# Kernel tuning notes

Hardware: AMD Instinct MI355X
Metric: run time of the kernel (lower is better)

The kernel has to match this reference:

```python
import jax, jax.numpy as jnp
import numpy as np

N_EMBD = 1024
HEAD_SIZE = 128
B, T = 8, 4096


def setup_inputs() -> dict:
    key = jax.random.key(0)
    ks = jax.random.split(key, 7)
    s = 1.0 / np.sqrt(N_EMBD)
    return {
        "x": jax.random.normal(ks[0], (B, T, N_EMBD), dtype=jnp.float32),
        "Wq": jax.random.uniform(ks[1], (N_EMBD, HEAD_SIZE), jnp.float32, -s, s),
        "bq": jax.random.uniform(ks[2], (HEAD_SIZE,), jnp.float32, -s, s),
        "Wk": jax.random.uniform(ks[3], (N_EMBD, HEAD_SIZE), jnp.float32, -s, s),
        "bk": jax.random.uniform(ks[4], (HEAD_SIZE,), jnp.float32, -s, s),
        "Wv": jax.random.uniform(ks[5], (N_EMBD, HEAD_SIZE), jnp.float32, -s, s),
        "bv": jax.random.uniform(ks[6], (HEAD_SIZE,), jnp.float32, -s, s),
    }


def reference(x, Wq, bq, Wk, bk, Wv, bv):
    # q,k,v: [B,T,H]
    q = x @ Wq + bq
    k = x @ Wk + bk
    v = x @ Wv + bv
    scale = HEAD_SIZE ** -0.5
    att = jnp.einsum("bth,bsh->bts", q, k) * scale  # [B,T,T]
    t = x.shape[1]
    causal = jnp.tril(jnp.ones((t, t), dtype=bool))
    att = jnp.where(causal, att, -jnp.inf)
    att = jax.nn.softmax(att, axis=-1)
    # dropout with p=0.0 is identity (eval-mode equivalent)
    out = jnp.einsum("bts,bsh->bth", att, v)  # [B,T,H]
    return out
```

## Files before the change

### kernel.cpp

```cpp
#include <hip/hip_runtime.h>
#include <hip/hip_bf16.h>
#include <stdint.h>

#define BATCH 8
#define SEQ   4096
#define EMB   1024
#define HD    128
#define NROWS 32768

typedef __attribute__((ext_vector_type(8))) short short8;
typedef __attribute__((ext_vector_type(4))) float f32x4;

__device__ inline unsigned short f2bf(float f) {
    union { float f; unsigned int u; } c; c.f = f;
    unsigned int u = c.u;
    unsigned int r = (u + 0x7fffu + ((u >> 16) & 1u)) >> 16;
    return (unsigned short)r;
}
__device__ inline float bf2f(unsigned short u) {
    union { unsigned int i; float f; } c; c.i = ((unsigned int)u) << 16; return c.f;
}
__device__ inline unsigned int pkbf(float a, float b) {
    __hip_bfloat162 h = __float22bfloat162_rn(make_float2(a, b));
    union { __hip_bfloat162 h; unsigned int u; } c; c.h = h; return c.u;
}

#define GLDS16(gp, lp) __builtin_amdgcn_global_load_lds( \
    (const __attribute__((address_space(1))) void*)(gp), \
    (__attribute__((address_space(3))) void*)(lp), 16, 0, 0)

__device__ inline void decomp(int it, int& b, int& qt, int& kv) {
    b = it / 1056;
    int r = it - b * 1056;
    int q = (int)((__builtin_sqrtf(4.0f * (float)r + 1.0f) - 1.0f) * 0.5f);
    while ((q + 1) * (q + 2) <= r) ++q;
    while (q * (q + 1) > r) --q;
    qt = q;
    kv = r - q * (q + 1);
}
__device__ inline int chunk_of(int I) {
    return (I < 4352) ? (I / 17) : (256 + ((I - 4352) >> 4));
}
__device__ inline int base1(int qt) {
    if (qt < 8)  return qt;
    if (qt < 16) return 8 + 2 * (qt - 8);
    if (qt < 24) return 24 + 3 * (qt - 16);
    return 48 + 4 * (qt - 24);
}

__global__ __launch_bounds__(256) void prep_kernel(
    const float* __restrict__ Wq, const float* __restrict__ bq,
    const float* __restrict__ Wk, const float* __restrict__ bk,
    const float* __restrict__ Wv, const float* __restrict__ bv,
    unsigned short* __restrict__ wt, float* __restrict__ biasc)
{
    const int n = blockIdx.x;
    const int sel = n >> 7, h = n & 127;
    const float* W = (sel == 0) ? Wq : (sel == 1) ? Wk : Wv;
    const int tid = threadIdx.x;
    const int k0 = tid * 4;
    union { unsigned short us[4]; uint2 v; } pk;
#pragma unroll
    for (int u = 0; u < 4; ++u) pk.us[u] = f2bf(W[(size_t)(k0 + u) * HD + h]);
    *(uint2*)&wt[(size_t)n * EMB + k0] = pk.v;
    if (tid == 0) {
        const float* bp = (sel == 0) ? bq : (sel == 1) ? bk : bv;
        biasc[n] = bp[h];
    }
}

__global__ __launch_bounds__(768, 3) void gemm_qkv(
    const float* __restrict__ x, const unsigned short* __restrict__ wt,
    const float* __restrict__ biasc,
    unsigned short* __restrict__ q, unsigned short* __restrict__ kOut,
    unsigned short* __restrict__ vt)
{
    const int m0  = blockIdx.x * 128;
    const int tid = threadIdx.x;
    const int wave = tid >> 6, lane = tid & 63;
    const int quad = lane >> 4, l15 = lane & 15;
    const int wm = (wave >= 6) ? 1 : 0;
    const int wn = wave - wm * 6;

    __shared__ __align__(16) unsigned short As[2][128][40];
    __shared__ __align__(16) unsigned short Bs[2][12288];

    f32x4 acc[4][4];
#pragma unroll
    for (int i = 0; i < 4; ++i)
#pragma unroll
        for (int j = 0; j < 4; ++j) acc[i][j] = (f32x4){0.f, 0.f, 0.f, 0.f};

    const int aactive = (tid < 512);
    const int arow = tid >> 3, akc = (tid & 7) * 4;
    float4 aR0, aR1;

#define LOAD_A(kt)                                                          \
    if (aactive) {                                                          \
        aR0 = *(const float4*)(x + (size_t)(m0 + arow) * EMB + (kt) * 32 + akc);        \
        aR1 = *(const float4*)(x + (size_t)(m0 + arow + 64) * EMB + (kt) * 32 + akc);   \
    }
#define WRITE_A(buf)                                                        \
    if (aactive) {                                                          \
        union { unsigned short us[4]; uint2 v; } p0, p1;                    \
        p0.us[0] = f2bf(aR0.x); p0.us[1] = f2bf(aR0.y);                     \
        p0.us[2] = f2bf(aR0.z); p0.us[3] = f2bf(aR0.w);                     \
        *(uint2*)&As[buf][arow][akc] = p0.v;                                \
        p1.us[0] = f2bf(aR1.x); p1.us[1] = f2bf(aR1.y);                     \
        p1.us[2] = f2bf(aR1.z); p1.us[3] = f2bf(aR1.w);                     \
        *(uint2*)&As[buf][arow + 64][akc] = p1.v;                           \
    }
#define STAGE_B(kt, buf)                                                    \
    {                                                                       \
        _Pragma("unroll")                                                   \
        for (int g = 0; g < 2; ++g) {                                       \
            int s0 = (g * 12 + wave) * 64;                                  \
            int s  = s0 + lane;                                             \
            int n  = s >> 2, c = (s & 3) ^ (n & 3);                         \
            GLDS16(wt + (size_t)n * EMB + (kt) * 32 + c * 8,                \
                   &Bs[buf][s0 * 8]);                                       \
        }                                                                   \
    }

    LOAD_A(0); STAGE_B(0, 0); WRITE_A(0);
    int cur = 0;

    for (int kt = 0; kt < 32; ++kt) {
        __syncthreads();
        if (kt < 31) { LOAD_A(kt + 1); STAGE_B(kt + 1, cur ^ 1); }
        short8 af[4], bw[4];
#pragma unroll
        for (int mj = 0; mj < 4; ++mj)
            af[mj] = *(const short8*)&As[cur][wm * 64 + mj * 16 + l15][quad * 8];
#pragma unroll
        for (int ni = 0; ni < 4; ++ni) {
            int n = wn * 64 + ni * 16 + l15;
            bw[ni] = *(const short8*)&Bs[cur][n * 32 + ((quad ^ (n & 3)) << 3)];
        }
#pragma unroll
        for (int ni = 0; ni < 4; ++ni)
#pragma unroll
            for (int mj = 0; mj < 4; ++mj)
                acc[ni][mj] = __builtin_amdgcn_mfma_f32_16x16x32_bf16(
                    bw[ni], af[mj], acc[ni][mj], 0, 0, 0);
        if (kt < 31) WRITE_A(cur ^ 1);
        cur ^= 1;
    }

    const float qscale = 0.08838834764831845f * 1.4426950408889634f;
    const int bb = m0 >> 12;
    const int t0 = m0 & 4095;
    const int mrow0 = m0 + wm * 64;
    const int tl0   = t0 + wm * 64;
#pragma unroll
    for (int ni = 0; ni < 4; ++ni) {
        int colbase = wn * 64 + ni * 16;
        int sel = colbase >> 7;
        int c0 = colbase + quad * 4;
        float4 bv4 = *(const float4*)&biasc[c0];
#pragma unroll
        for (int mj = 0; mj < 4; ++mj) {
            int m = mrow0 + mj * 16 + l15;
            if (sel == 0) {
                union { unsigned short us[4]; uint2 v; } pk;
#pragma unroll
                for (int j = 0; j < 4; ++j)
                    pk.us[j] = f2bf((acc[ni][mj][j] + ((const float*)&bv4)[j]) * qscale);
                *(uint2*)&q[(size_t)m * HD + (c0 & 127)] = pk.v;
            } else if (sel == 1) {
                union { unsigned short us[4]; uint2 v; } pk;
#pragma unroll
                for (int j = 0; j < 4; ++j)
                    pk.us[j] = f2bf(acc[ni][mj][j] + ((const float*)&bv4)[j]);
                *(uint2*)&kOut[(size_t)m * HD + (c0 & 127)] = pk.v;
            } else {
#pragma unroll
                for (int j = 0; j < 4; ++j) {
                    int h = (c0 & 127) + j;
                    vt[((size_t)(bb * 128 + h)) * SEQ + tl0 + mj * 16 + l15] =
                        f2bf(acc[ni][mj][j] + ((const float*)&bv4)[j]);
                }
            }
        }
    }
#undef LOAD_A
#undef WRITE_A
#undef STAGE_B
}

__global__ __launch_bounds__(256, 2) void attn_kernel(
    const unsigned short* __restrict__ q, const unsigned short* __restrict__ k,
    const unsigned short* __restrict__ vt, float* __restrict__ out,
    float* __restrict__ Oseg, float2* __restrict__ ml)
{
    const int rank  = blockIdx.x;
    const int start = (rank < 256) ? 17 * rank : 4352 + ((rank - 256) << 4);
    const int iend  = start + ((rank < 256) ? 17 : 16);

    const int tid  = threadIdx.x;
    const int wave = tid >> 6, lane = tid & 63;
    const int quad = lane >> 4, l15 = lane & 15;

    __shared__ __align__(16) unsigned short Ks[2][8192];
    __shared__ __align__(16) unsigned short Vs[2][8192];

    const int bpa0 = (l15 + 16 * ((2 * quad) & 3)) * 4;
    const int bpa1 = (l15 + 16 * ((2 * quad + 1) & 3)) * 4;

#define STAGE_KV(b_, kv_, buf_)                                              \
    {                                                                        \
        const size_t kb0 = (size_t)(b_) * SEQ + (kv_) * 64;                  \
        const size_t vb0 = (size_t)(b_) * HD * SEQ + (kv_) * 64;             \
        _Pragma("unroll")                                                    \
        for (int g = 0; g < 4; ++g) {                                        \
            int s0 = (g * 4 + wave) * 64;                                    \
            int s  = s0 + lane;                                              \
            int key = s >> 4, c = (s & 15) ^ (key & 15);                     \
            GLDS16(k + (kb0 + key) * HD + c * 8, &Ks[buf_][s0 * 8]);         \
        }                                                                    \
        _Pragma("unroll")                                                    \
        for (int g = 0; g < 4; ++g) {                                        \
            int s0 = (g * 4 + wave) * 64;                                    \
            int s  = s0 + lane;                                              \
            int h = s >> 3, c = (s & 7) ^ (h & 7);                           \
            GLDS16(vt + vb0 + (size_t)h * SEQ + c * 8, &Vs[buf_][s0 * 8]);   \
        }                                                                    \
    }

    int b, qt, kv;
    decomp(start, b, qt, kv);

    short8 qf[2][4];
    f32x4  o[2][8];
    float  m_r[2], l_r[2];
    int    qrow0 = 0;

#define CTX_INIT(b_, q_)                                                     \
    {                                                                        \
        qrow0 = (q_) * 128 + wave * 32;                                      \
        const size_t qoff = (size_t)(b_) * SEQ + qrow0;                      \
        _Pragma("unroll")                                                    \
        for (int mi = 0; mi < 2; ++mi)                                       \
            _Pragma("unroll")                                                \
            for (int kh = 0; kh < 4; ++kh)                                   \
                qf[mi][kh] = *(const short8*)(q + (qoff + mi * 16 + l15) * HD + kh * 32 + quad * 8); \
        _Pragma("unroll")                                                    \
        for (int mi = 0; mi < 2; ++mi) {                                     \
            _Pragma("unroll")                                                \
            for (int hi = 0; hi < 8; ++hi) o[mi][hi] = (f32x4){0.f, 0.f, 0.f, 0.f}; \
            m_r[mi] = -1e30f; l_r[mi] = 0.f;                                 \
        }                                                                    \
    }

#define CTX_FLUSH()                                                          \
    {                                                                        \
        const int I0 = b * 1056 + qt * (qt + 1);                             \
        const int j  = rank - chunk_of(I0);                                  \
        const int rr = wave * 32;                                            \
        float* obase;                                                        \
        if (j == 0) obase = out + ((size_t)b * SEQ + qrow0) * HD;            \
        else obase = Oseg + ((size_t)(b * 80 + base1(qt) + j - 1) * 128 + rr) * HD; \
        const size_t mlb = ((size_t)(b * 32 + qt) * 5 + j) * 128 + rr;       \
        _Pragma("unroll")                                                    \
        for (int mi = 0; mi < 2; ++mi) {                                     \
            if (quad == 0) ml[mlb + mi * 16 + l15] = make_float2(m_r[mi], l_r[mi]); \
            _Pragma("unroll")                                                \
            for (int hi = 0; hi < 8; ++hi)                                   \
                *(f32x4*)&obase[(size_t)(mi * 16 + l15) * HD + hi * 16 + quad * 4] = o[mi][hi]; \
        }                                                                    \
    }

    STAGE_KV(b, kv, 0);
    CTX_INIT(b, qt);
    int cur = 0;

    for (int it = start; it < iend; ++it) {
        int b2 = 0, qt2 = 0, kv2 = 0;
        const bool more = (it + 1 < iend);
        if (more) decomp(it + 1, b2, qt2, kv2);

        __syncthreads();
        if (more) STAGE_KV(b2, kv2, cur ^ 1);

        const int key0 = kv * 64;
        f32x4 s[2][4];
#pragma unroll
        for (int mi = 0; mi < 2; ++mi)
#pragma unroll
            for (int ni = 0; ni < 4; ++ni) s[mi][ni] = (f32x4){0.f, 0.f, 0.f, 0.f};
        __builtin_amdgcn_s_setprio(1);
#pragma unroll
        for (int kh = 0; kh < 4; ++kh) {
#pragma unroll
            for (int ni = 0; ni < 4; ++ni) {
                short8 kf = *(const short8*)&Ks[cur][(ni * 16 + l15) * 128 + (((kh * 4 + quad) ^ l15) << 3)];
                s[0][ni] = __builtin_amdgcn_mfma_f32_16x16x32_bf16(kf, qf[0][kh], s[0][ni], 0, 0, 0);
                s[1][ni] = __builtin_amdgcn_mfma_f32_16x16x32_bf16(kf, qf[1][kh], s[1][ni], 0, 0, 0);
            }
        }
        __builtin_amdgcn_s_setprio(0);
        if (key0 + 63 > qrow0) {
#pragma unroll
            for (int mi = 0; mi < 2; ++mi)
#pragma unroll
                for (int ni = 0; ni < 4; ++ni)
#pragma unroll
                    for (int j = 0; j < 4; ++j) {
                        int key = key0 + ni * 16 + quad * 4 + j;
                        int t   = qrow0 + mi * 16 + l15;
                        if (key > t) s[mi][ni][j] = -1e30f;
                    }
        }
        unsigned int pk[2][4][2];
#pragma unroll
        for (int mi = 0; mi < 2; ++mi) {
            float mx = -1e30f;
#pragma unroll
            for (int ni = 0; ni < 4; ++ni)
#pragma unroll
                for (int j = 0; j < 4; ++j) mx = fmaxf(mx, s[mi][ni][j]);
            mx = fmaxf(mx, __shfl_xor(mx, 16));
            mx = fmaxf(mx, __shfl_xor(mx, 32));
            if (!__all(mx - m_r[mi] <= 8.0f)) {
                float mnew = fmaxf(m_r[mi], mx);
                float alpha = __builtin_amdgcn_exp2f(m_r[mi] - mnew);
                m_r[mi] = mnew;
                l_r[mi] *= alpha;
#pragma unroll
                for (int hi = 0; hi < 8; ++hi) o[mi][hi] *= alpha;
            }
            const float mcur = m_r[mi];
            float rs = 0.f;
#pragma unroll
            for (int ni = 0; ni < 4; ++ni) {
                float p0 = __builtin_amdgcn_exp2f(s[mi][ni][0] - mcur);
                float p1 = __builtin_amdgcn_exp2f(s[mi][ni][1] - mcur);
                float p2 = __builtin_amdgcn_exp2f(s[mi][ni][2] - mcur);
                float p3 = __builtin_amdgcn_exp2f(s[mi][ni][3] - mcur);
                rs += (p0 + p1) + (p2 + p3);
                pk[mi][ni][0] = pkbf(p0, p1);
                pk[mi][ni][1] = pkbf(p2, p3);
            }
            rs += __shfl_xor(rs, 16);
            rs += __shfl_xor(rs, 32);
            l_r[mi] += rs;
        }
        short8 pT[2][2];
#pragma unroll
        for (int mi = 0; mi < 2; ++mi)
#pragma unroll
            for (int sk = 0; sk < 2; ++sk) {
                union { unsigned int u[4]; short8 s8; } pt;
                int lo = 2 * sk, hi_ = 2 * sk + 1;
                unsigned int a0 = (unsigned)__builtin_amdgcn_ds_bpermute(bpa0, (int)pk[mi][lo][0]);
                unsigned int b0 = (unsigned)__builtin_amdgcn_ds_bpermute(bpa0, (int)pk[mi][hi_][0]);
                pt.u[0] = (quad < 2) ? a0 : b0;
                unsigned int a1 = (unsigned)__builtin_amdgcn_ds_bpermute(bpa0, (int)pk[mi][lo][1]);
                unsigned int b1 = (unsigned)__builtin_amdgcn_ds_bpermute(bpa0, (int)pk[mi][hi_][1]);
                pt.u[1] = (quad < 2) ? a1 : b1;
                unsigned int a2 = (unsigned)__builtin_amdgcn_ds_bpermute(bpa1, (int)pk[mi][lo][0]);
                unsigned int b2 = (unsigned)__builtin_amdgcn_ds_bpermute(bpa1, (int)pk[mi][hi_][0]);
                pt.u[2] = (quad < 2) ? a2 : b2;
                unsigned int a3 = (unsigned)__builtin_amdgcn_ds_bpermute(bpa1, (int)pk[mi][lo][1]);
                unsigned int b3 = (unsigned)__builtin_amdgcn_ds_bpermute(bpa1, (int)pk[mi][hi_][1]);
                pt.u[3] = (quad < 2) ? a3 : b3;
                pT[mi][sk] = pt.s8;
            }
        __builtin_amdgcn_s_setprio(1);
#pragma unroll
        for (int sk = 0; sk < 2; ++sk)
#pragma unroll
            for (int hi = 0; hi < 8; ++hi) {
                short8 vf = *(const short8*)&Vs[cur][(hi * 16 + l15) * 64 + (((sk * 4 + quad) ^ (l15 & 7)) << 3)];
                o[0][hi] = __builtin_amdgcn_mfma_f32_16x16x32_bf16(vf, pT[0][sk], o[0][hi], 0, 0, 0);
                o[1][hi] = __builtin_amdgcn_mfma_f32_16x16x32_bf16(vf, pT[1][sk], o[1][hi], 0, 0, 0);
            }
        __builtin_amdgcn_s_setprio(0);

        if (kv == 2 * qt + 1 || !more) {
            CTX_FLUSH();
            if (more && kv == 2 * qt + 1) CTX_INIT(b2, qt2);
        }
        b = b2; qt = qt2; kv = kv2;
        cur ^= 1;
    }
#undef STAGE_KV
#undef CTX_INIT
#undef CTX_FLUSH
}

__global__ __launch_bounds__(256) void merge_kernel(
    float* __restrict__ out, const float* __restrict__ Oseg,
    const float2* __restrict__ ml)
{
    int idx = blockIdx.x * 256 + threadIdx.x;
    int row = idx >> 5;
    int hc  = (idx & 31) << 2;
    int b = row >> 12, t = row & 4095, qt = t >> 7, rr = t & 127;
    int I0  = b * 1056 + qt * (qt + 1);
    int nkv = 2 * (qt + 1);
    int c_lo = chunk_of(I0);
    int c_hi = chunk_of(I0 + nkv - 1);
    int nseg = c_hi - c_lo + 1;

    const float2* mlp = ml + ((size_t)(b * 32 + qt) * 5) * 128 + rr;
    float2 s0 = mlp[0];
    float M = s0.x;
    for (int j = 1; j < nseg; ++j) M = fmaxf(M, mlp[(size_t)j * 128].x);

    float w0 = __builtin_amdgcn_exp2f(s0.x - M);
    float L  = w0 * s0.y;
    f32x4 a = *(const f32x4*)&out[(size_t)row * HD + hc];
    a = a * w0;
    for (int j = 1; j < nseg; ++j) {
        float2 mj = mlp[(size_t)j * 128];
        float w = __builtin_amdgcn_exp2f(mj.x - M);
        L += w * mj.y;
        const float* sp = Oseg + ((size_t)(b * 80 + base1(qt) + j - 1) * 128 + rr) * HD + hc;
        f32x4 sv = *(const f32x4*)sp;
        a = a + sv * w;
    }
    float inv = 1.0f / L;
    *(f32x4*)&out[(size_t)row * HD + hc] = a * inv;
}

extern "C" void kernel_launch(void* const* d_in, const int* in_sizes, int n_in,
                              void* d_out, int out_size, void* d_ws, size_t ws_size,
                              hipStream_t stream) {
    const float* x  = (const float*)d_in[0];
    const float* Wq = (const float*)d_in[1];
    const float* bq = (const float*)d_in[2];
    const float* Wk = (const float*)d_in[3];
    const float* bk = (const float*)d_in[4];
    const float* Wv = (const float*)d_in[5];
    const float* bv = (const float*)d_in[6];
    float* out = (float*)d_out;

    unsigned short* wt    = (unsigned short*)d_ws;
    float*          biasc = (float*)((char*)d_ws + 786432);
    unsigned short* qb    = (unsigned short*)((char*)d_ws + 787968);
    unsigned short* kb    = qb  + (size_t)NROWS * HD;
    unsigned short* vtb   = kb  + (size_t)NROWS * HD;
    float*          Oseg  = (float*)((char*)d_ws + 787968 + 3ull * NROWS * HD * 2);
    float2*         mlseg = (float2*)((char*)Oseg + 640ull * 128 * HD * 4);

    prep_kernel<<<dim3(384), 256, 0, stream>>>(Wq, bq, Wk, bk, Wv, bv, wt, biasc);
    gemm_qkv<<<dim3(256), 768, 0, stream>>>(x, wt, biasc, qb, kb, vtb);
    attn_kernel<<<dim3(512), 256, 0, stream>>>(qb, kb, vtb, out, Oseg, mlseg);
    merge_kernel<<<dim3(NROWS * 32 / 256), 256, 0, stream>>>(out, Oseg, mlseg);
}
```

Before: 316.8 us.

## Halve KV tile to 32 keys and split causal attention across 768 blocks

The attention kernel now walks K/V in 32-key tiles instead of 64. The flattened work is redistributed into 768 equal chunks of 22 tiles, interleaved across block indices, with three blocks per CU allowed by launch bounds and half-size LDS buffers. Waves whose 32 query rows lie entirely before a key tile now skip that tile's compute, which trims masked work on diagonal tiles. In exchange each tile carries more sync and staging overhead, and the extra partial segments add work to the merge pass and to workspace traffic.

```diff
diff --git a/kernel.cpp b/kernel.cpp
--- a/kernel.cpp
+++ b/kernel.cpp
@@ -30,22 +30,21 @@
     (__attribute__((address_space(3))) void*)(lp), 16, 0, 0)
 
 __device__ inline void decomp(int it, int& b, int& qt, int& kv) {
-    b = it / 1056;
-    int r = it - b * 1056;
-    int q = (int)((__builtin_sqrtf(4.0f * (float)r + 1.0f) - 1.0f) * 0.5f);
-    while ((q + 1) * (q + 2) <= r) ++q;
-    while (q * (q + 1) > r) --q;
+    b = it / 2112;
+    int r = it - b * 2112;
+    int q = (int)((__builtin_sqrtf(2.0f * (float)r + 1.0f) - 1.0f) * 0.5f);
+    while (2 * (q + 1) * (q + 2) <= r) ++q;
+    while (2 * q * (q + 1) > r) --q;
     qt = q;
-    kv = r - q * (q + 1);
-}
-__device__ inline int chunk_of(int I) {
-    return (I < 4352) ? (I / 17) : (256 + ((I - 4352) >> 4));
+    kv = r - 2 * q * (q + 1);
 }
 __device__ inline int base1(int qt) {
-    if (qt < 8)  return qt;
-    if (qt < 16) return 8 + 2 * (qt - 8);
-    if (qt < 24) return 24 + 3 * (qt - 16);
-    return 48 + 4 * (qt - 24);
+    if (qt < 5)  return qt;
+    if (qt < 11) return 5 + 2 * (qt - 5);
+    if (qt < 16) return 17 + 3 * (qt - 11);
+    if (qt < 22) return 32 + 4 * (qt - 16);
+    if (qt < 27) return 56 + 5 * (qt - 22);
+    return 81 + 6 * (qt - 27);
 }
 
 __global__ __launch_bounds__(256) void prep_kernel(
@@ -188,41 +187,42 @@
 #undef STAGE_B
 }
 
-__global__ __launch_bounds__(256, 2) void attn_kernel(
+__global__ __launch_bounds__(256, 3) void attn_kernel(
     const unsigned short* __restrict__ q, const unsigned short* __restrict__ k,
     const unsigned short* __restrict__ vt, float* __restrict__ out,
     float* __restrict__ Oseg, float2* __restrict__ ml)
 {
     const int rank  = blockIdx.x;
-    const int start = (rank < 256) ? 17 * rank : 4352 + ((rank - 256) << 4);
-    const int iend  = start + ((rank < 256) ? 17 : 16);
+    const int chunk = (rank & 7) * 96 + (rank >> 3);
+    const int start = chunk * 22;
+    const int iend  = start + 22;
 
     const int tid  = threadIdx.x;
     const int wave = tid >> 6, lane = tid & 63;
     const int quad = lane >> 4, l15 = lane & 15;
 
-    __shared__ __align__(16) unsigned short Ks[2][8192];
-    __shared__ __align__(16) unsigned short Vs[2][8192];
+    __shared__ __align__(16) unsigned short Ks[2][4096];
+    __shared__ __align__(16) unsigned short Vs[2][4096];
 
     const int bpa0 = (l15 + 16 * ((2 * quad) & 3)) * 4;
     const int bpa1 = (l15 + 16 * ((2 * quad + 1) & 3)) * 4;
 
 #define STAGE_KV(b_, kv_, buf_)                                              \
     {                                                                        \
-        const size_t kb0 = (size_t)(b_) * SEQ + (kv_) * 64;                  \
-        const size_t vb0 = (size_t)(b_) * HD * SEQ + (kv_) * 64;             \
+        const size_t kb0 = (size_t)(b_) * SEQ + (kv_) * 32;                  \
+        const size_t vb0 = (size_t)(b_) * HD * SEQ + (kv_) * 32;             \
         _Pragma("unroll")                                                    \
-        for (int g = 0; g < 4; ++g) {                                        \
+        for (int g = 0; g < 2; ++g) {                                        \
             int s0 = (g * 4 + wave) * 64;                                    \
             int s  = s0 + lane;                                              \
             int key = s >> 4, c = (s & 15) ^ (key & 15);                     \
             GLDS16(k + (kb0 + key) * HD + c * 8, &Ks[buf_][s0 * 8]);         \
         }                                                                    \
         _Pragma("unroll")                                                    \
-        for (int g = 0; g < 4; ++g) {                                        \
+        for (int g = 0; g < 2; ++g) {                                        \
             int s0 = (g * 4 + wave) * 64;                                    \
             int s  = s0 + lane;                                              \
-            int h = s >> 3, c = (s & 7) ^ (h & 7);                           \
+            int h = s >> 2, c = (s & 3) ^ ((h >> 2) & 3);                    \
             GLDS16(vt + vb0 + (size_t)h * SEQ + c * 8, &Vs[buf_][s0 * 8]);   \
         }                                                                    \
     }
@@ -254,13 +254,13 @@
 
 #define CTX_FLUSH()                                                          \
     {                                                                        \
-        const int I0 = b * 1056 + qt * (qt + 1);                             \
-        const int j  = rank - chunk_of(I0);                                  \
+        const int I0 = b * 2112 + 2 * qt * (qt + 1);                         \
+        const int j  = chunk - I0 / 22;                                      \
         const int rr = wave * 32;                                            \
         float* obase;                                                        \
         if (j == 0) obase = out + ((size_t)b * SEQ + qrow0) * HD;            \
-        else obase = Oseg + ((size_t)(b * 80 + base1(qt) + j - 1) * 128 + rr) * HD; \
-        const size_t mlb = ((size_t)(b * 32 + qt) * 5 + j) * 128 + rr;       \
+        else obase = Oseg + ((size_t)(b * 112 + base1(qt) + j - 1) * 128 + rr) * HD; \
+        const size_t mlb = ((size_t)(b * 32 + qt) * 7 + j) * 128 + rr;       \
         _Pragma("unroll")                                                    \
         for (int mi = 0; mi < 2; ++mi) {                                     \
             if (quad == 0) ml[mlb + mi * 16 + l15] = make_float2(m_r[mi], l_r[mi]); \
@@ -282,104 +282,101 @@
         __syncthreads();
         if (more) STAGE_KV(b2, kv2, cur ^ 1);
 
-        const int key0 = kv * 64;
-        f32x4 s[2][4];
-#pragma unroll
-        for (int mi = 0; mi < 2; ++mi)
-#pragma unroll
-            for (int ni = 0; ni < 4; ++ni) s[mi][ni] = (f32x4){0.f, 0.f, 0.f, 0.f};
-        __builtin_amdgcn_s_setprio(1);
-#pragma unroll
-        for (int kh = 0; kh < 4; ++kh) {
-#pragma unroll
-            for (int ni = 0; ni < 4; ++ni) {
-                short8 kf = *(const short8*)&Ks[cur][(ni * 16 + l15) * 128 + (((kh * 4 + quad) ^ l15) << 3)];
-                s[0][ni] = __builtin_amdgcn_mfma_f32_16x16x32_bf16(kf, qf[0][kh], s[0][ni], 0, 0, 0);
-                s[1][ni] = __builtin_amdgcn_mfma_f32_16x16x32_bf16(kf, qf[1][kh], s[1][ni], 0, 0, 0);
-            }
+        const int key0 = kv * 32;
+        if (key0 <= qrow0 + 31) {
+            f32x4 s[2][2];
+#pragma unroll
+            for (int mi = 0; mi < 2; ++mi)
+#pragma unroll
+                for (int ni = 0; ni < 2; ++ni) s[mi][ni] = (f32x4){0.f, 0.f, 0.f, 0.f};
+            __builtin_amdgcn_s_setprio(1);
+#pragma unroll
+            for (int kh = 0; kh < 4; ++kh) {
+#pragma unroll
+                for (int ni = 0; ni < 2; ++ni) {
+                    short8 kf = *(const short8*)&Ks[cur][(ni * 16 + l15) * 128 + (((kh * 4 + quad) ^ l15) << 3)];
+                    s[0][ni] = __builtin_amdgcn_mfma_f32_16x16x32_bf16(kf, qf[0][kh], s[0][ni], 0, 0, 0);
+                    s[1][ni] = __builtin_amdgcn_mfma_f32_16x16x32_bf16(kf, qf[1][kh], s[1][ni], 0, 0, 0);
+                }
+            }
+            __builtin_amdgcn_s_setprio(0);
+            if (key0 + 31 > qrow0) {
+#pragma unroll
+                for (int mi = 0; mi < 2; ++mi)
+#pragma unroll
+                    for (int ni = 0; ni < 2; ++ni)
+#pragma unroll
+                        for (int j = 0; j < 4; ++j) {
+                            int key = key0 + ni * 16 + quad * 4 + j;
+                            int t   = qrow0 + mi * 16 + l15;
+                            if (key > t) s[mi][ni][j] = -1e30f;
+                        }
+            }
+            unsigned int pk[2][2][2];
+#pragma unroll
+            for (int mi = 0; mi < 2; ++mi) {
+                float mx = -1e30f;
+#pragma unroll
+                for (int ni = 0; ni < 2; ++ni)
+#pragma unroll
+                    for (int j = 0; j < 4; ++j) mx = fmaxf(mx, s[mi][ni][j]);
+                mx = fmaxf(mx, __shfl_xor(mx, 16));
+                mx = fmaxf(mx, __shfl_xor(mx, 32));
+                if (!__all(mx - m_r[mi] <= 8.0f)) {
+                    float mnew = fmaxf(m_r[mi], mx);
+                    float alpha = __builtin_amdgcn_exp2f(m_r[mi] - mnew);
+                    m_r[mi] = mnew;
+                    l_r[mi] *= alpha;
+#pragma unroll
+                    for (int hi = 0; hi < 8; ++hi) o[mi][hi] *= alpha;
+                }
+                const float mcur = m_r[mi];
+                float rs = 0.f;
+#pragma unroll
+                for (int ni = 0; ni < 2; ++ni) {
+                    float p0 = __builtin_amdgcn_exp2f(s[mi][ni][0] - mcur);
+                    float p1 = __builtin_amdgcn_exp2f(s[mi][ni][1] - mcur);
+                    float p2 = __builtin_amdgcn_exp2f(s[mi][ni][2] - mcur);
+                    float p3 = __builtin_amdgcn_exp2f(s[mi][ni][3] - mcur);
+                    rs += (p0 + p1) + (p2 + p3);
+                    pk[mi][ni][0] = pkbf(p0, p1);
+                    pk[mi][ni][1] = pkbf(p2, p3);
+                }
+                rs += __shfl_xor(rs, 16);
+                rs += __shfl_xor(rs, 32);
+                l_r[mi] += rs;
+            }
+            short8 pT[2];
+#pragma unroll
+            for (int mi = 0; mi < 2; ++mi) {
+                union { unsigned int u[4]; short8 s8; } pt;
+                unsigned int a0 = (unsigned)__builtin_amdgcn_ds_bpermute(bpa0, (int)pk[mi][0][0]);
+                unsigned int b0 = (unsigned)__builtin_amdgcn_ds_bpermute(bpa0, (int)pk[mi][1][0]);
+                pt.u[0] = (quad < 2) ? a0 : b0;
+                unsigned int a1 = (unsigned)__builtin_amdgcn_ds_bpermute(bpa0, (int)pk[mi][0][1]);
+                unsigned int b1 = (unsigned)__builtin_amdgcn_ds_bpermute(bpa0, (int)pk[mi][1][1]);
+                pt.u[1] = (quad < 2) ? a1 : b1;
+                unsigned int a2 = (unsigned)__builtin_amdgcn_ds_bpermute(bpa1, (int)pk[mi][0][0]);
+                unsigned int b2 = (unsigned)__builtin_amdgcn_ds_bpermute(bpa1, (int)pk[mi][1][0]);
+                pt.u[2] = (quad < 2) ? a2 : b2;
+                unsigned int a3 = (unsigned)__builtin_amdgcn_ds_bpermute(bpa1, (int)pk[mi][0][1]);
+                unsigned int b3 = (unsigned)__builtin_amdgcn_ds_bpermute(bpa1, (int)pk[mi][1][1]);
+                pt.u[3] = (quad < 2) ? a3 : b3;
+                pT[mi] = pt.s8;
+            }
+            __builtin_amdgcn_s_setprio(1);
+#pragma unroll
+            for (int hi = 0; hi < 8; ++hi) {
+                short8 vf = *(const short8*)&Vs[cur][(hi * 16 + l15) * 32 + ((quad ^ (l15 >> 2)) << 3)];
+                o[0][hi] = __builtin_amdgcn_mfma_f32_16x16x32_bf16(vf, pT[0], o[0][hi], 0, 0, 0);
+                o[1][hi] = __builtin_amdgcn_mfma_f32_16x16x32_bf16(vf, pT[1], o[1][hi], 0, 0, 0);
+            }
+            __builtin_amdgcn_s_setprio(0);
         }
-        __builtin_amdgcn_s_setprio(0);
-        if (key0 + 63 > qrow0) {
-#pragma unroll
-            for (int mi = 0; mi < 2; ++mi)
-#pragma unroll
-                for (int ni = 0; ni < 4; ++ni)
-#pragma unroll
-                    for (int j = 0; j < 4; ++j) {
-                        int key = key0 + ni * 16 + quad * 4 + j;
-                        int t   = qrow0 + mi * 16 + l15;
-                        if (key > t) s[mi][ni][j] = -1e30f;
-                    }
-        }
-        unsigned int pk[2][4][2];
-#pragma unroll
-        for (int mi = 0; mi < 2; ++mi) {
-            float mx = -1e30f;
-#pragma unroll
-            for (int ni = 0; ni < 4; ++ni)
-#pragma unroll
-                for (int j = 0; j < 4; ++j) mx = fmaxf(mx, s[mi][ni][j]);
-            mx = fmaxf(mx, __shfl_xor(mx, 16));
-            mx = fmaxf(mx, __shfl_xor(mx, 32));
-            if (!__all(mx - m_r[mi] <= 8.0f)) {
-                float mnew = fmaxf(m_r[mi], mx);
-                float alpha = __builtin_amdgcn_exp2f(m_r[mi] - mnew);
-                m_r[mi] = mnew;
-                l_r[mi] *= alpha;
-#pragma unroll
-                for (int hi = 0; hi < 8; ++hi) o[mi][hi] *= alpha;
-            }
-            const float mcur = m_r[mi];
-            float rs = 0.f;
-#pragma unroll
-            for (int ni = 0; ni < 4; ++ni) {
-                float p0 = __builtin_amdgcn_exp2f(s[mi][ni][0] - mcur);
-                float p1 = __builtin_amdgcn_exp2f(s[mi][ni][1] - mcur);
-                float p2 = __builtin_amdgcn_exp2f(s[mi][ni][2] - mcur);
-                float p3 = __builtin_amdgcn_exp2f(s[mi][ni][3] - mcur);
-                rs += (p0 + p1) + (p2 + p3);
-                pk[mi][ni][0] = pkbf(p0, p1);
-                pk[mi][ni][1] = pkbf(p2, p3);
-            }
-            rs += __shfl_xor(rs, 16);
-            rs += __shfl_xor(rs, 32);
-            l_r[mi] += rs;
-        }
-        short8 pT[2][2];
-#pragma unroll
-        for (int mi = 0; mi < 2; ++mi)
-#pragma unroll
-            for (int sk = 0; sk < 2; ++sk) {
-                union { unsigned int u[4]; short8 s8; } pt;
-                int lo = 2 * sk, hi_ = 2 * sk + 1;
-                unsigned int a0 = (unsigned)__builtin_amdgcn_ds_bpermute(bpa0, (int)pk[mi][lo][0]);
-                unsigned int b0 = (unsigned)__builtin_amdgcn_ds_bpermute(bpa0, (int)pk[mi][hi_][0]);
-                pt.u[0] = (quad < 2) ? a0 : b0;
-                unsigned int a1 = (unsigned)__builtin_amdgcn_ds_bpermute(bpa0, (int)pk[mi][lo][1]);
-                unsigned int b1 = (unsigned)__builtin_amdgcn_ds_bpermute(bpa0, (int)pk[mi][hi_][1]);
-                pt.u[1] = (quad < 2) ? a1 : b1;
-                unsigned int a2 = (unsigned)__builtin_amdgcn_ds_bpermute(bpa1, (int)pk[mi][lo][0]);
-                unsigned int b2 = (unsigned)__builtin_amdgcn_ds_bpermute(bpa1, (int)pk[mi][hi_][0]);
-                pt.u[2] = (quad < 2) ? a2 : b2;
-                unsigned int a3 = (unsigned)__builtin_amdgcn_ds_bpermute(bpa1, (int)pk[mi][lo][1]);
-                unsigned int b3 = (unsigned)__builtin_amdgcn_ds_bpermute(bpa1, (int)pk[mi][hi_][1]);
-                pt.u[3] = (quad < 2) ? a3 : b3;
-                pT[mi][sk] = pt.s8;
-            }
-        __builtin_amdgcn_s_setprio(1);
-#pragma unroll
-        for (int sk = 0; sk < 2; ++sk)
-#pragma unroll
-            for (int hi = 0; hi < 8; ++hi) {
-                short8 vf = *(const short8*)&Vs[cur][(hi * 16 + l15) * 64 + (((sk * 4 + quad) ^ (l15 & 7)) << 3)];
-                o[0][hi] = __builtin_amdgcn_mfma_f32_16x16x32_bf16(vf, pT[0][sk], o[0][hi], 0, 0, 0);
-                o[1][hi] = __builtin_amdgcn_mfma_f32_16x16x32_bf16(vf, pT[1][sk], o[1][hi], 0, 0, 0);
-            }
-        __builtin_amdgcn_s_setprio(0);
-
-        if (kv == 2 * qt + 1 || !more) {
+
+        if (kv == 4 * qt + 3 || !more) {
             CTX_FLUSH();
-            if (more && kv == 2 * qt + 1) CTX_INIT(b2, qt2);
+            if (more && kv == 4 * qt + 3) CTX_INIT(b2, qt2);
         }
         b = b2; qt = qt2; kv = kv2;
         cur ^= 1;
@@ -397,13 +394,11 @@
     int row = idx >> 5;
     int hc  = (idx & 31) << 2;
     int b = row >> 12, t = row & 4095, qt = t >> 7, rr = t & 127;
-    int I0  = b * 1056 + qt * (qt + 1);
-    int nkv = 2 * (qt + 1);
-    int c_lo = chunk_of(I0);
-    int c_hi = chunk_of(I0 + nkv - 1);
-    int nseg = c_hi - c_lo + 1;
-
-    const float2* mlp = ml + ((size_t)(b * 32 + qt) * 5) * 128 + rr;
+    int I0   = b * 2112 + 2 * qt * (qt + 1);
+    int n    = 4 * (qt + 1);
+    int nseg = (I0 + n - 1) / 22 - I0 / 22 + 1;
+
+    const float2* mlp = ml + ((size_t)(b * 32 + qt) * 7) * 128 + rr;
     float2 s0 = mlp[0];
     float M = s0.x;
     for (int j = 1; j < nseg; ++j) M = fmaxf(M, mlp[(size_t)j * 128].x);
@@ -416,7 +411,7 @@
         float2 mj = mlp[(size_t)j * 128];
         float w = __builtin_amdgcn_exp2f(mj.x - M);
         L += w * mj.y;
-        const float* sp = Oseg + ((size_t)(b * 80 + base1(qt) + j - 1) * 128 + rr) * HD + hc;
+        const float* sp = Oseg + ((size_t)(b * 112 + base1(qt) + j - 1) * 128 + rr) * HD + hc;
         f32x4 sv = *(const f32x4*)sp;
         a = a + sv * w;
     }
@@ -442,10 +437,10 @@
     unsigned short* kb    = qb  + (size_t)NROWS * HD;
     unsigned short* vtb   = kb  + (size_t)NROWS * HD;
     float*          Oseg  = (float*)((char*)d_ws + 787968 + 3ull * NROWS * HD * 2);
-    float2*         mlseg = (float2*)((char*)Oseg + 640ull * 128 * HD * 4);
+    float2*         mlseg = (float2*)((char*)Oseg + 896ull * 128 * HD * 4);
 
     prep_kernel<<<dim3(384), 256, 0, stream>>>(Wq, bq, Wk, bk, Wv, bv, wt, biasc);
     gemm_qkv<<<dim3(256), 768, 0, stream>>>(x, wt, biasc, qb, kb, vtb);
-    attn_kernel<<<dim3(512), 256, 0, stream>>>(qb, kb, vtb, out, Oseg, mlseg);
+    attn_kernel<<<dim3(768), 256, 0, stream>>>(qb, kb, vtb, out, Oseg, mlseg);
     merge_kernel<<<dim3(NROWS * 32 / 256), 256, 0, stream>>>(out, Oseg, mlseg);
 }
```

New measurement: 308.6 us. 2.6% less time.
